# Performance work log

Hardware: AMD Instinct MI355X
Metric: run time of the kernel (lower is better)

## Reference

```python
import jax, jax.numpy as jnp
import numpy as np

N, E, B = 16384, 65536, 32
D_IN, ED, H, L = 4, 5, 64, 3  # node feat, edge feat, hidden=output, num layers
NEG_SLOPE = 0.1
EPS = 1e-5


def _leaky(v):
    return jnp.where(v > 0, v, NEG_SLOPE * v)


def setup_inputs() -> dict:
    key = jax.random.key(0)
    ks = jax.random.split(key, 32)
    s = 0.05
    inp = {
        'x': jax.random.normal(ks[0], (N, D_IN), jnp.float32),
        'edge_index': jax.random.randint(ks[1], (2, E), 0, N),
        'edge_attr': jax.random.normal(ks[2], (E, ED), jnp.float32),
        'batch': jnp.sort(jax.random.randint(ks[3], (N,), 0, B)),
        # input projection Linear(4 -> H)
        'W_in': s * jax.random.normal(ks[4], (H, D_IN), jnp.float32),
        'b_in': jnp.zeros((H,), jnp.float32),
        # per-layer edge MLP: Linear(ED->H), Linear(H->H), Linear(H->H*H); stacked over L
        'ew1': s * jax.random.normal(ks[5], (L, H, ED), jnp.float32),
        'eb1': jnp.zeros((L, H), jnp.float32),
        'ew2': s * jax.random.normal(ks[6], (L, H, H), jnp.float32),
        'eb2': jnp.zeros((L, H), jnp.float32),
        'ew3': s * jax.random.normal(ks[7], (L, H * H, H), jnp.float32),
        'eb3': jnp.zeros((L, H * H), jnp.float32),
        # NNConv root weight + bias per layer
        'root_w': s * jax.random.normal(ks[8], (L, H, H), jnp.float32),
        'root_b': jnp.zeros((L, H), jnp.float32),
        # LayerNorm per layer
        'ln_g': jnp.ones((L, H), jnp.float32),
        'ln_b': jnp.zeros((L, H), jnp.float32),
        # prediction head: Linear(H->H), Linear(H->H//2), Linear(H//2->1)
        'pw1': s * jax.random.normal(ks[9], (H, H), jnp.float32),
        'pb1': jnp.zeros((H,), jnp.float32),
        'pw2': s * jax.random.normal(ks[10], (H // 2, H), jnp.float32),
        'pb2': jnp.zeros((H // 2,), jnp.float32),
        'pw3': s * jax.random.normal(ks[11], (1, H // 2), jnp.float32),
        'pb3': jnp.zeros((1,), jnp.float32),
    }
    return inp


def reference(x, edge_index, edge_attr, batch, W_in, b_in, ew1, eb1, ew2, eb2,
              ew3, eb3, root_w, root_b, ln_g, ln_b, pw1, pb1, pw2, pb2, pw3, pb3):
    src, dst = edge_index[0], edge_index[1]
    n_nodes = x.shape[0]
    n_edges = edge_attr.shape[0]
    # in-degree for scatter-mean (PyG yields 0 for isolated nodes)
    deg = jax.ops.segment_sum(jnp.ones((n_edges,), x.dtype), dst, num_segments=n_nodes)
    deg = jnp.maximum(deg, 1.0)[:, None]

    # input projection (dropout = identity in eval)
    h = _leaky(x @ W_in.T + b_in)

    for l in range(L):
        # edge MLP -> per-edge weight matrix [E, H, H]
        e = _leaky(edge_attr @ ew1[l].T + eb1[l])
        e = _leaky(e @ ew2[l].T + eb2[l])
        Wf = (e @ ew3[l].T + eb3[l]).reshape(n_edges, H, H)
        # message = x_src @ W_edge, scatter-mean to dst
        msg = jnp.einsum('ei,eio->eo', h[src], Wf)
        agg = jax.ops.segment_sum(msg, dst, num_segments=n_nodes) / deg
        out = agg + h @ root_w[l].T + root_b[l]
        # LayerNorm (post-norm)
        mu = out.mean(-1, keepdims=True)
        var = ((out - mu) ** 2).mean(-1, keepdims=True)
        out = (out - mu) * jax.lax.rsqrt(var + EPS) * ln_g[l] + ln_b[l]
        # activation + (identity) dropout + residual (in==out for all layers)
        h = _leaky(out) + h

    # global mean pool over graphs
    pooled = jax.ops.segment_sum(h, batch, num_segments=B)
    cnt = jax.ops.segment_sum(jnp.ones((n_nodes,), h.dtype), batch, num_segments=B)
    pooled = pooled / jnp.maximum(cnt, 1.0)[:, None]

    # prediction head
    p = _leaky(pooled @ pw1.T + pb1)
    p = _leaky(p @ pw2.T + pb2)
    pred = (p @ pw3.T + pb3).squeeze(-1)  # [B]
    return pred
```

## Files before the change

### kernel.cpp

```cpp
#include <hip/hip_runtime.h>
#include <hip/hip_bf16.h>

#define N_NODES 16384
#define N_EDGES 65536
#define NB      32
#define H       64
#define NLAYERS 3
#define NEG     0.1f
#define LN_EPS  1e-5f

typedef _Float16 f16;
typedef _Float16 f16x2 __attribute__((ext_vector_type(2)));
typedef _Float16 f16x8 __attribute__((ext_vector_type(8)));
typedef __fp16   hf16x2 __attribute__((ext_vector_type(2)));
typedef float    f32x16 __attribute__((ext_vector_type(16)));

union F16x8 { f16x8 v; f16x2 p[4]; int4 i4; int2 i2[2]; };
union F16x2U { f16x2 h2; hf16x2 raw; unsigned int u; };
union F16U   { f16 h; unsigned short u; };

__device__ __forceinline__ f16x2 pkrtz(float a, float b) {
    F16x2U t; t.raw = __builtin_amdgcn_cvt_pkrtz(a, b); return t.h2;
}
__device__ __forceinline__ float leaky(float v) { return v > 0.f ? v : NEG * v; }

__global__ __launch_bounds__(256) void k_setup(const float* __restrict__ x,
                                               const float* __restrict__ Win,
                                               const float* __restrict__ bin,
                                               const int* __restrict__ dst,
                                               const float* __restrict__ ew3,
                                               const float* __restrict__ eb3,
                                               float* __restrict__ h,
                                               float* __restrict__ deg,
                                               f16* __restrict__ Bp) {
    int bid = blockIdx.x;
    if (bid < 4096) {
        int t = bid * 256 + threadIdx.x;
        int n = t >> 6, j = t & 63;
        const float* xr = x + n * 4;
        const float* wr = Win + j * 4;
        float v = bin[j] + xr[0] * wr[0] + xr[1] * wr[1] + xr[2] * wr[2] + xr[3] * wr[3];
        h[t] = leaky(v);
    } else if (bid < 4352) {
        int e = (bid - 4096) * 256 + threadIdx.x;
        atomicAdd(&deg[dst[e]], 1.0f);
    } else {
        int tg    = (bid - 4352) * 256 + threadIdx.x;
        int lane  = tg & 63;
        int gslot = tg >> 6;
        int l     = gslot / 520;
        int slot  = gslot - l * 520;
        const float* ew3l = ew3 + (size_t)l * 262144;
        const float* eb3l = eb3 + (size_t)l * 4096;
        int i   = slot >> 3;
        int rem = slot & 7;
        int ks  = rem >> 1;
        int oq  = rem & 1;
        int o   = oq * 32 + (lane & 31);
        int k0  = ks * 16 + (lane >> 5) * 8;
        float v[8];
        if (i < 64) {
            const float* s = ew3l + ((size_t)(i * 64 + o)) * 64 + k0;
            float4 a = ((const float4*)s)[0];
            float4 b = ((const float4*)s)[1];
            v[0] = a.x; v[1] = a.y; v[2] = a.z; v[3] = a.w;
            v[4] = b.x; v[5] = b.y; v[6] = b.z; v[7] = b.w;
        } else {
#pragma unroll
            for (int j = 0; j < 8; j++) v[j] = eb3l[(k0 + j) * 64 + o];
        }
        union { int4 i4; f16 a[8]; } out;
#pragma unroll
        for (int j = 0; j < 8; j++) out.a[j] = (f16)v[j];
        *(int4*)(Bp + (size_t)l * 266240 + (size_t)slot * 512 + lane * 8) = out.i4;
    }
}

#define HS_STRIDE 76

__device__ __forceinline__ void loadB8c(const f16* __restrict__ Bp, int c, int lane, F16x8* dstB) {
    const f16* base = Bp + (((size_t)(c * 8)) << 9) + lane * 8;
#pragma unroll
    for (int s = 0; s < 8; s++)
        dstB[s].i4 = *(const int4*)(base + (s << 9));
}

__device__ __forceinline__ void msg_chunk1(const F16x8* __restrict__ B,
                                           f16x2 hb,
                                           const f16x2 (*e2p)[4], f32x16* CC) {
#pragma unroll
    for (int ks = 0; ks < 4; ks++) {
        F16x8 A;
#pragma unroll
        for (int r = 0; r < 4; r++) A.p[r] = hb * e2p[ks][r];
        int ch = (ks & 1) * 2;
        CC[ch + 0] = __builtin_amdgcn_mfma_f32_32x32x16_f16(A.v, B[ks * 2 + 0].v, CC[ch + 0], 0, 0, 0);
        CC[ch + 1] = __builtin_amdgcn_mfma_f32_32x32x16_f16(A.v, B[ks * 2 + 1].v, CC[ch + 1], 0, 0, 0);
    }
}

__global__ __launch_bounds__(256, 2) void k_msg(const float* __restrict__ h,
                                                const float* __restrict__ ea,
                                                const float* __restrict__ w1,
                                                const float* __restrict__ b1,
                                                const float* __restrict__ w2,
                                                const float* __restrict__ b2,
                                                const f16* __restrict__ Bp,
                                                const int* __restrict__ src,
                                                const int* __restrict__ dst,
                                                float* __restrict__ agg) {
    __shared__ __align__(16) unsigned short hsL[128 * HS_STRIDE];
    __shared__ __align__(16) unsigned short e1L[128 * 72];
    __shared__ __align__(16) unsigned short e2L[128 * 72];
    __shared__ float eas[128 * 8];
    __shared__ int dstL[128];

    const int t    = threadIdx.x;
    const int lane = t & 63;
    const int w    = t >> 6;
    const int eh   = w >> 1, oq = w & 1;
    const int m    = lane & 31;
    const int kp   = lane >> 5;
    const int eb   = blockIdx.x * 128;

    for (int idx = t; idx < 640; idx += 256) {
        int r = idx / 5, d = idx - r * 5;
        eas[r * 8 + d] = ea[(size_t)eb * 5 + idx];
    }
    {
        int e    = t >> 1;
        int half = t & 1;
        int nsrc = src[eb + e];
        const float4* hr = (const float4*)(h + (size_t)nsrc * 64 + half * 32);
        unsigned int* hrow = (unsigned int*)hsL + e * (HS_STRIDE / 2) + half * 16;
#pragma unroll
        for (int q = 0; q < 8; q++) {
            float4 v = hr[q];
            F16x2U p0, p1;
            p0.raw = __builtin_amdgcn_cvt_pkrtz(v.x, v.y);
            p1.raw = __builtin_amdgcn_cvt_pkrtz(v.z, v.w);
            hrow[q * 2 + 0] = p0.u;
            hrow[q * 2 + 1] = p1.u;
        }
        if (t < 128) dstL[t] = dst[eb + t];
    }
    __syncthreads();

    {
        int kk = t & 63;
        int eg = t >> 6;
        float w1r[5];
#pragma unroll
        for (int d = 0; d < 5; d++) w1r[d] = w1[kk * 5 + d];
        float b1r = b1[kk];
#pragma unroll 4
        for (int g = 0; g < 32; g++) {
            int row = eg * 32 + g;
            float4 a4 = *(const float4*)(eas + row * 8);
            float a5 = eas[row * 8 + 4];
            float v = b1r + a4.x * w1r[0] + a4.y * w1r[1] + a4.z * w1r[2] + a4.w * w1r[3] + a5 * w1r[4];
            F16U z; z.h = (f16)leaky(v);
            e1L[row * 72 + kk] = z.u;
        }
    }
    __syncthreads();

    {
        F16x8 W2f[4];
#pragma unroll
        for (int ks = 0; ks < 4; ks++) {
            const float* s = w2 + (size_t)(oq * 32 + m) * 64 + ks * 16 + kp * 8;
            float4 a = ((const float4*)s)[0];
            float4 b = ((const float4*)s)[1];
            W2f[ks].p[0] = pkrtz(a.x, a.y);
            W2f[ks].p[1] = pkrtz(a.z, a.w);
            W2f[ks].p[2] = pkrtz(b.x, b.y);
            W2f[ks].p[3] = pkrtz(b.z, b.w);
        }
        float b2r = b2[oq * 32 + m];
#pragma unroll
        for (int tt = 0; tt < 2; tt++) {
            f32x16 C2 = {0,0,0,0,0,0,0,0,0,0,0,0,0,0,0,0};
#pragma unroll
            for (int ks = 0; ks < 4; ks++) {
                F16x8 A;
                A.i4 = *(const int4*)(e1L + (size_t)((eh * 2 + tt) * 32 + m) * 72 + ks * 16 + kp * 8);
                C2 = __builtin_amdgcn_mfma_f32_32x32x16_f16(A.v, W2f[ks].v, C2, 0, 0, 0);
            }
#pragma unroll
            for (int reg = 0; reg < 16; reg++) {
                int r = (reg & 3) + 8 * (reg >> 2) + 4 * kp;
                F16U z; z.h = (f16)leaky(C2[reg] + b2r);
                e2L[((eh * 2 + tt) * 32 + r) * 72 + oq * 32 + m] = z.u;
            }
        }
    }
    __syncthreads();

    const int tt = w;
    f16x2 e2p[4][4];
#pragma unroll
    for (int ks = 0; ks < 4; ks++) {
        F16x8 q;
        q.i4 = *(const int4*)(e2L + (size_t)(tt * 32 + m) * 72 + ks * 16 + kp * 8);
        e2p[ks][0] = q.p[0]; e2p[ks][1] = q.p[1];
        e2p[ks][2] = q.p[2]; e2p[ks][3] = q.p[3];
    }

    f32x16 CC[4];
#pragma unroll
    for (int q = 0; q < 4; q++)
#pragma unroll
        for (int r = 0; r < 16; r++) CC[q][r] = 0.f;

    const unsigned short* hp = hsL + (tt * 32 + m) * HS_STRIDE;

    F16x8 B0[8], B1[8];
    loadB8c(Bp, 0, lane, B0);
    loadB8c(Bp, 1, lane, B1);
    for (int it = 0; it < 31; it++) {
        unsigned int rr = *(const unsigned int*)(hp + 2 * it);
        F16x2U h0, h1;
        h0.u = __builtin_amdgcn_perm(rr, rr, 0x01000100u);
        h1.u = __builtin_amdgcn_perm(rr, rr, 0x03020302u);
        msg_chunk1(B0, h0.h2, e2p, CC);  loadB8c(Bp, 2 * it + 2, lane, B0);
        msg_chunk1(B1, h1.h2, e2p, CC);  loadB8c(Bp, 2 * it + 3, lane, B1);
    }
    {
        unsigned int rr = *(const unsigned int*)(hp + 62);
        F16x2U h0, h1;
        h0.u = __builtin_amdgcn_perm(rr, rr, 0x01000100u);
        h1.u = __builtin_amdgcn_perm(rr, rr, 0x03020302u);
        msg_chunk1(B0, h0.h2, e2p, CC);  loadB8c(Bp, 64, lane, B0);
        msg_chunk1(B1, h1.h2, e2p, CC);
    }

#pragma unroll
    for (int ks = 0; ks < 4; ks++) {
        int koff = (ks * 16 + kp * 8) * 2;
        const char* rp = (const char*)hsL + (size_t)(tt * 32 + m) * (HS_STRIDE * 2) + koff;
        F16x8 A;
        A.i2[0] = *(const int2*)(rp); A.i2[1] = *(const int2*)(rp + 8);
        int ch = (ks & 1) * 2;
        CC[ch + 0] = __builtin_amdgcn_mfma_f32_32x32x16_f16(A.v, B0[ks * 2 + 0].v, CC[ch + 0], 0, 0, 0);
        CC[ch + 1] = __builtin_amdgcn_mfma_f32_32x32x16_f16(A.v, B0[ks * 2 + 1].v, CC[ch + 1], 0, 0, 0);
    }

#pragma unroll
    for (int reg = 0; reg < 16; reg++) {
        int r = (reg & 3) + 8 * (reg >> 2) + 4 * kp;
        float* basep = &agg[(size_t)dstL[tt * 32 + r] * 64];
        atomicAdd(basep + m,      CC[0][reg] + CC[2][reg]);
        atomicAdd(basep + 32 + m, CC[1][reg] + CC[3][reg]);
    }
}

__global__ __launch_bounds__(256) void k_node(const float* __restrict__ agg,
                                              const float* __restrict__ deg,
                                              const float* __restrict__ rw,
                                              const float* __restrict__ rb,
                                              const float* __restrict__ lg,
                                              const float* __restrict__ lb,
                                              float* __restrict__ h,
                                              const int* __restrict__ batch,
                                              float* __restrict__ pooled,
                                              int last) {
    __shared__ __align__(16) unsigned short hA[64 * 72];
    __shared__ float outL[64][68];
    int t = threadIdx.x;
    int nb = blockIdx.x * 64;
    int lane = t & 63, w = t >> 6;
    int nq = w >> 1, oq = w & 1;
    int m = lane & 31, kp = lane >> 5;

    {
        int r = t >> 2, c0 = (t & 3) * 16;
        const float4* hr = (const float4*)(h + (size_t)(nb + r) * 64 + c0);
        unsigned int* drow = (unsigned int*)hA + r * 36 + c0 / 2;
#pragma unroll
        for (int q = 0; q < 4; q++) {
            float4 v = hr[q];
            F16x2U p0, p1;
            p0.raw = __builtin_amdgcn_cvt_pkrtz(v.x, v.y);
            p1.raw = __builtin_amdgcn_cvt_pkrtz(v.z, v.w);
            drow[q * 2] = p0.u; drow[q * 2 + 1] = p1.u;
        }
    }
    F16x8 Bf[4];
#pragma unroll
    for (int ks = 0; ks < 4; ks++) {
        const float* s = rw + (size_t)(oq * 32 + m) * 64 + ks * 16 + kp * 8;
        float4 a = ((const float4*)s)[0];
        float4 b = ((const float4*)s)[1];
        Bf[ks].p[0] = pkrtz(a.x, a.y);
        Bf[ks].p[1] = pkrtz(a.z, a.w);
        Bf[ks].p[2] = pkrtz(b.x, b.y);
        Bf[ks].p[3] = pkrtz(b.z, b.w);
    }
    __syncthreads();

    f32x16 C = {0,0,0,0,0,0,0,0,0,0,0,0,0,0,0,0};
#pragma unroll
    for (int ks = 0; ks < 4; ks++) {
        F16x8 A;
        A.i4 = *(const int4*)(hA + (size_t)(nq * 32 + m) * 72 + ks * 16 + kp * 8);
        C = __builtin_amdgcn_mfma_f32_32x32x16_f16(A.v, Bf[ks].v, C, 0, 0, 0);
    }

    int o = oq * 32 + m;
#pragma unroll
    for (int reg = 0; reg < 16; reg++) {
        int r = (reg & 3) + 8 * (reg >> 2) + 4 * kp;
        int n = nq * 32 + r;
        outL[n][o] = C[reg] + rb[o] + agg[(size_t)(nb + n) * 64 + o] / fmaxf(deg[nb + n], 1.0f);
    }
    __syncthreads();

    float gj = lg[lane], bj = lb[lane];
    float accp = 0.f;
    int cur = batch[nb + w * 16];
    for (int q = 0; q < 16; q++) {
        int n = w * 16 + q;
        float v = outL[n][lane];
        float mu = v;
#pragma unroll
        for (int msk = 32; msk > 0; msk >>= 1) mu += __shfl_xor(mu, msk);
        mu *= (1.f / 64.f);
        float d = v - mu;
        float var = d * d;
#pragma unroll
        for (int msk = 32; msk > 0; msk >>= 1) var += __shfl_xor(var, msk);
        var *= (1.f / 64.f);
        float ov = d * rsqrtf(var + LN_EPS) * gj + bj;
        float hn = leaky(ov) + h[(size_t)(nb + n) * 64 + lane];
        h[(size_t)(nb + n) * 64 + lane] = hn;
        if (last) {
            int b = batch[nb + n];
            if (b != cur) { atomicAdd(&pooled[cur * 64 + lane], accp); accp = 0.f; cur = b; }
            accp += hn;
        }
    }
    if (last) atomicAdd(&pooled[cur * 64 + lane], accp);
}

__global__ __launch_bounds__(256) void k_head(const float* __restrict__ pooled,
                                              const int* __restrict__ batch,
                                              const float* __restrict__ pw1, const float* __restrict__ pb1,
                                              const float* __restrict__ pw2, const float* __restrict__ pb2,
                                              const float* __restrict__ pw3, const float* __restrict__ pb3,
                                              float* __restrict__ out) {
    __shared__ float cntL[32];
    __shared__ float ps[32][64];
    __shared__ float p1[32][64];
    __shared__ float p2[32][32];
    int t = threadIdx.x;
    if (t < 32) cntL[t] = 0.f;
    __syncthreads();
    {
        const int4* bp4 = (const int4*)(batch + t * 64);
        int cur = batch[t * 64];
        float c = 0.f;
        for (int q = 0; q < 16; q++) {
            int4 b4 = bp4[q];
            int bs[4] = { b4.x, b4.y, b4.z, b4.w };
#pragma unroll
            for (int e = 0; e < 4; e++) {
                if (bs[e] != cur) { atomicAdd(&cntL[cur], c); cur = bs[e]; c = 0.f; }
                c += 1.f;
            }
        }
        atomicAdd(&cntL[cur], c);
    }
    __syncthreads();
    for (int idx = t; idx < 2048; idx += 256) {
        int b = idx >> 6, j = idx & 63;
        ps[b][j] = pooled[idx] / fmaxf(cntL[b], 1.0f);
    }
    __syncthreads();
    for (int idx = t; idx < 2048; idx += 256) {
        int b = idx >> 6, j = idx & 63;
        float v = pb1[j];
#pragma unroll 8
        for (int i = 0; i < 64; i++) v += ps[b][i] * pw1[j * 64 + i];
        p1[b][j] = leaky(v);
    }
    __syncthreads();
    for (int idx = t; idx < 1024; idx += 256) {
        int b = idx >> 5, j = idx & 31;
        float v = pb2[j];
#pragma unroll 8
        for (int i = 0; i < 64; i++) v += p1[b][i] * pw2[j * 64 + i];
        p2[b][j] = leaky(v);
    }
    __syncthreads();
    if (t < 32) {
        float v = pb3[0];
#pragma unroll 8
        for (int i = 0; i < 32; i++) v += p2[t][i] * pw3[i];
        out[t] = v;
    }
}

extern "C" void kernel_launch(void* const* d_in, const int* in_sizes, int n_in,
                              void* d_out, int out_size, void* d_ws, size_t ws_size,
                              hipStream_t stream) {
    const float* x    = (const float*)d_in[0];
    const int*   eidx = (const int*)  d_in[1];
    const float* ea   = (const float*)d_in[2];
    const int*   bat  = (const int*)  d_in[3];
    const float* Win  = (const float*)d_in[4];
    const float* bin  = (const float*)d_in[5];
    const float* ew1  = (const float*)d_in[6];
    const float* eb1  = (const float*)d_in[7];
    const float* ew2  = (const float*)d_in[8];
    const float* eb2  = (const float*)d_in[9];
    const float* ew3  = (const float*)d_in[10];
    const float* eb3  = (const float*)d_in[11];
    const float* rw   = (const float*)d_in[12];
    const float* rb   = (const float*)d_in[13];
    const float* lg   = (const float*)d_in[14];
    const float* lb   = (const float*)d_in[15];
    const float* pw1  = (const float*)d_in[16];
    const float* pb1  = (const float*)d_in[17];
    const float* pw2  = (const float*)d_in[18];
    const float* pb2  = (const float*)d_in[19];
    const float* pw3  = (const float*)d_in[20];
    const float* pb3  = (const float*)d_in[21];
    float* out = (float*)d_out;

    float* ws     = (float*)d_ws;
    float* h      = ws;
    float* agg    = ws + 1048576;
    float* deg    = ws + 4194304;
    float* pooled = ws + 4210688;
    f16*   Bp     = (f16*)(ws + 4212800);

    const int* srcp = eidx;
    const int* dstp = eidx + N_EDGES;

    (void)hipMemsetAsync(agg, 0, (size_t)3164224 * sizeof(float), stream);

    k_setup<<<4742, 256, 0, stream>>>(x, Win, bin, dstp, ew3, eb3, h, deg, Bp);

    for (int l = 0; l < NLAYERS; l++) {
        float* agg_l = agg + (size_t)l * N_NODES * H;
        k_msg <<<N_EDGES / 128, 256, 0, stream>>>(h, ea, ew1 + l * 320, eb1 + l * 64,
                                                  ew2 + l * 4096, eb2 + l * 64,
                                                  Bp + (size_t)l * 266240,
                                                  srcp, dstp, agg_l);
        k_node<<<N_NODES / 64, 256, 0, stream>>>(agg_l, deg, rw + l * 4096, rb + l * 64,
                                                 lg + l * 64, lb + l * 64, h,
                                                 bat, pooled, l == NLAYERS - 1 ? 1 : 0);
    }

    k_head<<<1, 256, 0, stream>>>(pooled, bat, pw1, pb1, pw2, pb2, pw3, pb3, out);
}
```

Baseline: 356.3 us.

## Split message kernel output columns across 8 waves and merge edge-MLP LDS buffers

After: 339.4 us. 1.05x faster.

```diff
diff --git a/kernel.cpp b/kernel.cpp
--- a/kernel.cpp
+++ b/kernel.cpp
@@ -78,28 +78,31 @@
 
 #define HS_STRIDE 76
 
-__device__ __forceinline__ void loadB8c(const f16* __restrict__ Bp, int c, int lane, F16x8* dstB) {
-    const f16* base = Bp + (((size_t)(c * 8)) << 9) + lane * 8;
-#pragma unroll
-    for (int s = 0; s < 8; s++)
-        dstB[s].i4 = *(const int4*)(base + (s << 9));
-}
-
-__device__ __forceinline__ void msg_chunk1(const F16x8* __restrict__ B,
-                                           f16x2 hb,
-                                           const f16x2 (*e2p)[4], f32x16* CC) {
+__device__ __forceinline__ void loadB4c(const f16* __restrict__ Bp, int i, int oq, int lane, F16x8* dstB) {
+    const f16* base = Bp + (((size_t)(i * 8 + oq)) << 9) + lane * 8;
+#pragma unroll
+    for (int ks = 0; ks < 4; ks++)
+        dstB[ks].i4 = *(const int4*)(base + ((ks * 2) << 9));
+}
+__device__ __forceinline__ void loadB4(const f16* __restrict__ Bp, int oq, int lane, F16x8* dstB) {
+    const f16* base = Bp + (((size_t)(512 + oq)) << 9) + lane * 8;
+#pragma unroll
+    for (int ks = 0; ks < 4; ks++)
+        dstB[ks].i4 = *(const int4*)(base + ((ks * 2) << 9));
+}
+
+__device__ __forceinline__ void msg_chunk1t(const F16x8* __restrict__ B, f16x2 hb,
+                                            const f16x2 (*e2p)[4], f32x16* C) {
 #pragma unroll
     for (int ks = 0; ks < 4; ks++) {
         F16x8 A;
 #pragma unroll
         for (int r = 0; r < 4; r++) A.p[r] = hb * e2p[ks][r];
-        int ch = (ks & 1) * 2;
-        CC[ch + 0] = __builtin_amdgcn_mfma_f32_32x32x16_f16(A.v, B[ks * 2 + 0].v, CC[ch + 0], 0, 0, 0);
-        CC[ch + 1] = __builtin_amdgcn_mfma_f32_32x32x16_f16(A.v, B[ks * 2 + 1].v, CC[ch + 1], 0, 0, 0);
-    }
-}
-
-__global__ __launch_bounds__(256, 2) void k_msg(const float* __restrict__ h,
+        *C = __builtin_amdgcn_mfma_f32_32x32x16_f16(A.v, B[ks].v, *C, 0, 0, 0);
+    }
+}
+
+__global__ __launch_bounds__(512, 4) void k_msg(const float* __restrict__ h,
                                                 const float* __restrict__ ea,
                                                 const float* __restrict__ w1,
                                                 const float* __restrict__ b1,
@@ -110,31 +113,25 @@
                                                 const int* __restrict__ dst,
                                                 float* __restrict__ agg) {
     __shared__ __align__(16) unsigned short hsL[128 * HS_STRIDE];
-    __shared__ __align__(16) unsigned short e1L[128 * 72];
-    __shared__ __align__(16) unsigned short e2L[128 * 72];
-    __shared__ float eas[128 * 8];
+    __shared__ __align__(16) unsigned short eL[128 * 72];
     __shared__ int dstL[128];
 
     const int t    = threadIdx.x;
     const int lane = t & 63;
     const int w    = t >> 6;
-    const int eh   = w >> 1, oq = w & 1;
+    const int tt   = w >> 1, oq = w & 1;
     const int m    = lane & 31;
     const int kp   = lane >> 5;
     const int eb   = blockIdx.x * 128;
 
-    for (int idx = t; idx < 640; idx += 256) {
-        int r = idx / 5, d = idx - r * 5;
-        eas[r * 8 + d] = ea[(size_t)eb * 5 + idx];
-    }
-    {
-        int e    = t >> 1;
-        int half = t & 1;
+    {
+        int e  = t >> 2;
+        int q4 = t & 3;
         int nsrc = src[eb + e];
-        const float4* hr = (const float4*)(h + (size_t)nsrc * 64 + half * 32);
-        unsigned int* hrow = (unsigned int*)hsL + e * (HS_STRIDE / 2) + half * 16;
-#pragma unroll
-        for (int q = 0; q < 8; q++) {
+        const float4* hr = (const float4*)(h + (size_t)nsrc * 64) + q4 * 4;
+        unsigned int* hrow = (unsigned int*)hsL + e * (HS_STRIDE / 2) + q4 * 8;
+#pragma unroll
+        for (int q = 0; q < 4; q++) {
             float4 v = hr[q];
             F16x2U p0, p1;
             p0.raw = __builtin_amdgcn_cvt_pkrtz(v.x, v.y);
@@ -144,23 +141,21 @@
         }
         if (t < 128) dstL[t] = dst[eb + t];
     }
-    __syncthreads();
 
     {
         int kk = t & 63;
-        int eg = t >> 6;
         float w1r[5];
 #pragma unroll
         for (int d = 0; d < 5; d++) w1r[d] = w1[kk * 5 + d];
         float b1r = b1[kk];
+        const float* ear = ea + (size_t)(eb + w * 16) * 5;
 #pragma unroll 4
-        for (int g = 0; g < 32; g++) {
-            int row = eg * 32 + g;
-            float4 a4 = *(const float4*)(eas + row * 8);
-            float a5 = eas[row * 8 + 4];
-            float v = b1r + a4.x * w1r[0] + a4.y * w1r[1] + a4.z * w1r[2] + a4.w * w1r[3] + a5 * w1r[4];
+        for (int g = 0; g < 16; g++) {
+            float a0 = ear[g * 5 + 0], a1 = ear[g * 5 + 1], a2 = ear[g * 5 + 2];
+            float a3 = ear[g * 5 + 3], a4 = ear[g * 5 + 4];
+            float v = b1r + a0 * w1r[0] + a1 * w1r[1] + a2 * w1r[2] + a3 * w1r[3] + a4 * w1r[4];
             F16U z; z.h = (f16)leaky(v);
-            e1L[row * 72 + kk] = z.u;
+            eL[(w * 16 + g) * 72 + kk] = z.u;
         }
     }
     __syncthreads();
@@ -178,61 +173,57 @@
             W2f[ks].p[3] = pkrtz(b.z, b.w);
         }
         float b2r = b2[oq * 32 + m];
-#pragma unroll
-        for (int tt = 0; tt < 2; tt++) {
-            f32x16 C2 = {0,0,0,0,0,0,0,0,0,0,0,0,0,0,0,0};
-#pragma unroll
-            for (int ks = 0; ks < 4; ks++) {
-                F16x8 A;
-                A.i4 = *(const int4*)(e1L + (size_t)((eh * 2 + tt) * 32 + m) * 72 + ks * 16 + kp * 8);
-                C2 = __builtin_amdgcn_mfma_f32_32x32x16_f16(A.v, W2f[ks].v, C2, 0, 0, 0);
-            }
-#pragma unroll
-            for (int reg = 0; reg < 16; reg++) {
-                int r = (reg & 3) + 8 * (reg >> 2) + 4 * kp;
-                F16U z; z.h = (f16)leaky(C2[reg] + b2r);
-                e2L[((eh * 2 + tt) * 32 + r) * 72 + oq * 32 + m] = z.u;
-            }
-        }
-    }
-    __syncthreads();
-
-    const int tt = w;
+        F16x8 A4[4];
+#pragma unroll
+        for (int ks = 0; ks < 4; ks++)
+            A4[ks].i4 = *(const int4*)(eL + (size_t)(tt * 32 + m) * 72 + ks * 16 + kp * 8);
+        __syncthreads();
+        f32x16 C2 = {0,0,0,0,0,0,0,0,0,0,0,0,0,0,0,0};
+#pragma unroll
+        for (int ks = 0; ks < 4; ks++)
+            C2 = __builtin_amdgcn_mfma_f32_32x32x16_f16(A4[ks].v, W2f[ks].v, C2, 0, 0, 0);
+#pragma unroll
+        for (int reg = 0; reg < 16; reg++) {
+            int r = (reg & 3) + 8 * (reg >> 2) + 4 * kp;
+            F16U z; z.h = (f16)leaky(C2[reg] + b2r);
+            eL[(tt * 32 + r) * 72 + oq * 32 + m] = z.u;
+        }
+    }
+    __syncthreads();
+
     f16x2 e2p[4][4];
 #pragma unroll
     for (int ks = 0; ks < 4; ks++) {
         F16x8 q;
-        q.i4 = *(const int4*)(e2L + (size_t)(tt * 32 + m) * 72 + ks * 16 + kp * 8);
+        q.i4 = *(const int4*)(eL + (size_t)(tt * 32 + m) * 72 + ks * 16 + kp * 8);
         e2p[ks][0] = q.p[0]; e2p[ks][1] = q.p[1];
         e2p[ks][2] = q.p[2]; e2p[ks][3] = q.p[3];
     }
 
-    f32x16 CC[4];
-#pragma unroll
-    for (int q = 0; q < 4; q++)
-#pragma unroll
-        for (int r = 0; r < 16; r++) CC[q][r] = 0.f;
+    f32x16 CC0, CC1;
+#pragma unroll
+    for (int r = 0; r < 16; r++) { CC0[r] = 0.f; CC1[r] = 0.f; }
 
     const unsigned short* hp = hsL + (tt * 32 + m) * HS_STRIDE;
 
-    F16x8 B0[8], B1[8];
-    loadB8c(Bp, 0, lane, B0);
-    loadB8c(Bp, 1, lane, B1);
+    F16x8 B0[4], B1[4];
+    loadB4c(Bp, 0, oq, lane, B0);
+    loadB4c(Bp, 1, oq, lane, B1);
     for (int it = 0; it < 31; it++) {
         unsigned int rr = *(const unsigned int*)(hp + 2 * it);
         F16x2U h0, h1;
         h0.u = __builtin_amdgcn_perm(rr, rr, 0x01000100u);
         h1.u = __builtin_amdgcn_perm(rr, rr, 0x03020302u);
-        msg_chunk1(B0, h0.h2, e2p, CC);  loadB8c(Bp, 2 * it + 2, lane, B0);
-        msg_chunk1(B1, h1.h2, e2p, CC);  loadB8c(Bp, 2 * it + 3, lane, B1);
+        msg_chunk1t(B0, h0.h2, e2p, &CC0);  loadB4c(Bp, 2 * it + 2, oq, lane, B0);
+        msg_chunk1t(B1, h1.h2, e2p, &CC1);  loadB4c(Bp, 2 * it + 3, oq, lane, B1);
     }
     {
         unsigned int rr = *(const unsigned int*)(hp + 62);
         F16x2U h0, h1;
         h0.u = __builtin_amdgcn_perm(rr, rr, 0x01000100u);
         h1.u = __builtin_amdgcn_perm(rr, rr, 0x03020302u);
-        msg_chunk1(B0, h0.h2, e2p, CC);  loadB8c(Bp, 64, lane, B0);
-        msg_chunk1(B1, h1.h2, e2p, CC);
+        msg_chunk1t(B0, h0.h2, e2p, &CC0);  loadB4(Bp, oq, lane, B0);
+        msg_chunk1t(B1, h1.h2, e2p, &CC1);
     }
 
 #pragma unroll
@@ -241,17 +232,14 @@
         const char* rp = (const char*)hsL + (size_t)(tt * 32 + m) * (HS_STRIDE * 2) + koff;
         F16x8 A;
         A.i2[0] = *(const int2*)(rp); A.i2[1] = *(const int2*)(rp + 8);
-        int ch = (ks & 1) * 2;
-        CC[ch + 0] = __builtin_amdgcn_mfma_f32_32x32x16_f16(A.v, B0[ks * 2 + 0].v, CC[ch + 0], 0, 0, 0);
-        CC[ch + 1] = __builtin_amdgcn_mfma_f32_32x32x16_f16(A.v, B0[ks * 2 + 1].v, CC[ch + 1], 0, 0, 0);
-    }
-
+        CC0 = __builtin_amdgcn_mfma_f32_32x32x16_f16(A.v, B0[ks].v, CC0, 0, 0, 0);
+    }
+
+    int o = oq * 32 + m;
 #pragma unroll
     for (int reg = 0; reg < 16; reg++) {
         int r = (reg & 3) + 8 * (reg >> 2) + 4 * kp;
-        float* basep = &agg[(size_t)dstL[tt * 32 + r] * 64];
-        atomicAdd(basep + m,      CC[0][reg] + CC[2][reg]);
-        atomicAdd(basep + 32 + m, CC[1][reg] + CC[3][reg]);
+        atomicAdd(&agg[(size_t)dstL[tt * 32 + r] * 64 + o], CC0[reg] + CC1[reg]);
     }
 }
 
@@ -444,7 +432,7 @@
 
     for (int l = 0; l < NLAYERS; l++) {
         float* agg_l = agg + (size_t)l * N_NODES * H;
-        k_msg <<<N_EDGES / 128, 256, 0, stream>>>(h, ea, ew1 + l * 320, eb1 + l * 64,
+        k_msg <<<N_EDGES / 128, 512, 0, stream>>>(h, ea, ew1 + l * 320, eb1 + l * 64,
                                                   ew2 + l * 4096, eb2 + l * 64,
                                                   Bp + (size_t)l * 266240,
                                                   srcp, dstp, agg_l);
```
